# Kernel optimization log

Hardware: AMD Instinct MI355X
Metric: run time of the kernel (lower is better)

## Reference

```python
import jax, jax.numpy as jnp
import numpy as np


def setup_inputs() -> dict:
    key = jax.random.key(0)
    ks = jax.random.split(key, 4)
    B, T, E, H = 4, 4096, 512, 64
    x = jax.random.normal(ks[0], (B, T, E), dtype=jnp.float32)
    s = 1.0 / np.sqrt(E)
    Wq = jax.random.normal(ks[1], (E, H), dtype=jnp.float32) * s
    Wk = jax.random.normal(ks[2], (E, H), dtype=jnp.float32) * s
    Wv = jax.random.normal(ks[3], (E, H), dtype=jnp.float32) * s
    bq = jnp.zeros((H,), dtype=jnp.float32)
    bk = jnp.zeros((H,), dtype=jnp.float32)
    bv = jnp.zeros((H,), dtype=jnp.float32)
    return {"x": x, "Wq": Wq, "bq": bq, "Wk": Wk, "bk": bk, "Wv": Wv, "bv": bv}


def reference(x, Wq, bq, Wk, bk, Wv, bv):
    # Single-head causal attention (masked=True path; dropout off / eval mode).
    B, T, E = x.shape
    H = Wq.shape[1]
    q = x @ Wq + bq                      # [B,T,H]
    k = x @ Wk + bk                      # [B,T,H]
    v = x @ Wv + bv                      # [B,T,H]
    scale = jnp.asarray(H, x.dtype) ** -0.5
    w = jnp.einsum('bqh,bkh->bqk', q, k) * scale   # [B,T,T]
    causal = jnp.tril(jnp.ones((T, T), dtype=bool))
    w = jnp.where(causal, w, jnp.asarray(-jnp.inf, w.dtype))
    w = jax.nn.softmax(w, axis=-1)
    out = jnp.einsum('bqk,bkh->bqh', w, v)          # [B,T,H]
    return out
```

## Files before the change

### kernel.cpp

```cpp
#include <hip/hip_runtime.h>
#include <math.h>

#define B_SZ   4
#define T_SEQ  4096
#define E_DIM  512
#define H_DIM  64
#define AW     8
#define XSTR   520
#define QSCALE 0.180336878f

typedef float f32x4 __attribute__((ext_vector_type(4)));
typedef short s16x4 __attribute__((ext_vector_type(4)));
typedef short s16x8 __attribute__((ext_vector_type(8)));
typedef unsigned int u32x4 __attribute__((ext_vector_type(4)));

static __device__ __forceinline__ unsigned short f2bf(float f) {
    union { float f; unsigned int u; } c; c.f = f;
    return (unsigned short)((c.u + 0x7fffu + ((c.u >> 16) & 1u)) >> 16);
}

static __device__ __forceinline__ float exp2f_hw(float x) {
    return __builtin_amdgcn_exp2f(x);
}

static __device__ __forceinline__ unsigned int pack_bf16(float a, float b) {
    unsigned int ua = __builtin_bit_cast(unsigned int, a) + 0x8000u;
    unsigned int ub = __builtin_bit_cast(unsigned int, b) + 0x8000u;
    return __builtin_amdgcn_perm(ub, ua, 0x07060302u);
}

__global__ __launch_bounds__(256) void wconv(
    const float* __restrict__ Wq, const float* __restrict__ Wk, const float* __restrict__ Wv,
    unsigned short* __restrict__ Wf)
{
    const int fid  = blockIdx.x * 256 + threadIdx.x;
    const int nt   = fid >> 10;
    const int kc32 = (fid >> 6) & 15;
    const int lane = fid & 63;
    const int l15  = lane & 15, g = lane >> 4;
    const int col  = nt * 16 + l15;
    const int m    = col >> 6, h = col & 63;
    const float* src = (m == 0) ? Wq : (m == 1) ? Wk : Wv;
    const float sc = (m == 0) ? QSCALE : 1.0f;
    const int k0 = kc32 * 32 + 4 * g;
    s16x8 o;
    #pragma unroll
    for (int j = 0; j < 4; ++j) {
        o[j]     = (short)f2bf(src[(k0 + j) * H_DIM + h] * sc);
        o[4 + j] = (short)f2bf(src[(k0 + 16 + j) * H_DIM + h] * sc);
    }
    *(s16x8*)(Wf + (long long)fid * 8) = o;
}

__global__ __launch_bounds__(256) void qkv_mfma(
    const float* __restrict__ x, const unsigned short* __restrict__ Wf,
    const float* __restrict__ bq, const float* __restrict__ bk, const float* __restrict__ bv,
    unsigned short* __restrict__ qf, unsigned short* __restrict__ kf,
    unsigned short* __restrict__ vf)
{
    __shared__ unsigned short Xf[16 * XSTR];
    __shared__ unsigned short Wout[192][20];

    const int t = threadIdx.x, wv = t >> 6, l = t & 63, l15 = l & 15, g = l >> 4;
    const long long row0 = (long long)blockIdx.x * 16;

    const float* xbase = x + row0 * E_DIM;
    #pragma unroll
    for (int i = 0; i < 8; ++i) {
        const int n = t + 256 * i;
        const int r = n >> 7;
        const int c = (n & 127) * 4;
        const f32x4 xv = *(const f32x4*)(xbase + r * E_DIM + c);
        const int kc32 = c >> 5, rem = c & 31;
        const int gg = (rem & 15) >> 2, half = rem >> 4;
        unsigned int* dst = (unsigned int*)&Xf[kc32 * XSTR + (r + 16 * gg) * 8 + half * 4];
        dst[0] = pack_bf16(xv[0], xv[1]);
        dst[1] = pack_bf16(xv[2], xv[3]);
    }
    __syncthreads();

    f32x4 acc[3];
    #pragma unroll
    for (int i = 0; i < 3; ++i) acc[i] = (f32x4){0.f, 0.f, 0.f, 0.f};

    #pragma unroll
    for (int kc32 = 0; kc32 < 16; ++kc32) {
        const s16x8 xf = *(const s16x8*)&Xf[kc32 * XSTR + l * 8];
        #pragma unroll
        for (int i = 0; i < 3; ++i) {
            const int nt = wv + 4 * i;
            const s16x8 wf = *(const s16x8*)(Wf + (long long)((nt * 16 + kc32) * 64 + l) * 8);
            acc[i] = __builtin_amdgcn_mfma_f32_16x16x32_bf16(wf, xf, acc[i], 0, 0, 0);
        }
    }

    #pragma unroll
    for (int i = 0; i < 3; ++i) {
        const int nt = wv + 4 * i;
        const float* bsrc = (i == 0) ? bq : (i == 1) ? bk : bv;
        const float bscale = (i == 0) ? QSCALE : 1.0f;
        const f32x4 bb = *(const f32x4*)(bsrc + wv * 16 + 4 * g);
        #pragma unroll
        for (int r = 0; r < 4; ++r)
            Wout[nt * 16 + 4 * g + r][l15] = f2bf(acc[i][r] + bb[r] * bscale);
    }
    __syncthreads();

    const long long qt = blockIdx.x;

    if (t < 128) {
        const int hc = t >> 6, ll = t & 63, p15 = ll & 15, pg = (ll >> 4);
        s16x8 o;
        #pragma unroll
        for (int j = 0; j < 4; ++j) {
            o[j]     = (short)Wout[32 * hc + 4 * pg + j][p15];
            o[4 + j] = (short)Wout[32 * hc + 16 + 4 * pg + j][p15];
        }
        *(s16x8*)(qf + qt * 1024 + hc * 512 + ll * 8) = o;
    } else {
        const int tt = t - 128, half = tt >> 6, ll = tt & 63, p15 = ll & 15, pg = (ll >> 4);
        s16x8 o;
        #pragma unroll
        for (int j = 0; j < 4; ++j) {
            o[j]     = (short)Wout[64 + 32 * half + 4 * pg + j][p15];
            o[4 + j] = (short)Wout[64 + 32 * half + 16 + 4 * pg + j][p15];
        }
        *(s16x8*)(kf + qt * 1024 + half * 512 + ll * 8) = o;
    }

    {
        const int hc = t >> 6, ll = t & 63, p15 = ll & 15, pg = (ll >> 4);
        const long long ktg = qt >> 2;
        const int half = (int)((qt >> 1) & 1), pi = (int)(qt & 1);
        s16x4 o;
        #pragma unroll
        for (int j = 0; j < 4; ++j) o[j] = (short)Wout[128 + hc * 16 + p15][4 * pg + j];
        *(s16x4*)(vf + ktg * 4096 + hc * 1024 + half * 512 + ll * 8 + pi * 4) = o;
    }
}

__global__ __launch_bounds__(512, 2) void attn(
    const unsigned short* __restrict__ qf,
    const unsigned short* __restrict__ kf,
    const unsigned short* __restrict__ vf,
    float* __restrict__ out)
{
    __shared__ float Osh[AW][64][33];
    __shared__ float msh[AW][32];
    __shared__ float lsh[AW][32];

    const int t = threadIdx.x, wv = t >> 6, l = t & 63, l15 = l & 15, g = l >> 4;

    const int bid = blockIdx.x;
    const int xcd = bid & 7;
    const int b   = xcd >> 1;
    const int u   = (bid >> 3) * 2 + (xcd & 1);

    const unsigned short* kfb = kf + (long long)b * 64 * 4096 + l * 8;
    const unsigned short* vfb = vf + (long long)b * 64 * 4096 + l * 8;

    for (int p = 0; p < 2; ++p) {
        const int qi = p ? u : (127 - u);
        const int q0 = qi * 32;
        const int adiag = (q0 + 31) >> 6;

        s16x8 Qf[2][2];
        #pragma unroll
        for (int s = 0; s < 2; ++s) {
            const unsigned short* qp = qf + ((long long)b * 256 + qi * 2 + s) * 1024 + l * 8;
            Qf[s][0] = *(const s16x8*)qp;
            Qf[s][1] = *(const s16x8*)(qp + 512);
        }

        f32x4 O[2][4];
        #pragma unroll
        for (int s = 0; s < 2; ++s)
            #pragma unroll
            for (int hc = 0; hc < 4; ++hc) O[s][hc] = (f32x4){0.f, 0.f, 0.f, 0.f};
        float m[2]   = {-INFINITY, -INFINITY};
        float lsm[2] = {0.f, 0.f};

        s16x8 Ka[4], Kc[4];
        #define LOAD_K(KT, A, C)                                              \
            {                                                                 \
                const unsigned short* p_ = kfb + (long long)(KT) * 4096;      \
                _Pragma("unroll")                                             \
                for (int ks = 0; ks < 4; ++ks) {                              \
                    (A)[ks] = *(const s16x8*)(p_ + ks * 1024);                \
                    (C)[ks] = *(const s16x8*)(p_ + ks * 1024 + 512);          \
                }                                                             \
            }

        if (wv <= adiag) LOAD_K(wv, Ka, Kc);

        for (int kt = wv; kt <= adiag; kt += AW) {
            const int ktb = kt * 64;
            const f32x4 z = {0.f, 0.f, 0.f, 0.f};

            f32x4 S[2][4];
            __builtin_amdgcn_s_setprio(1);
            #pragma unroll
            for (int ks = 0; ks < 4; ++ks) {
                #pragma unroll
                for (int s = 0; s < 2; ++s) {
                    f32x4 s0 = __builtin_amdgcn_mfma_f32_16x16x32_bf16(Ka[ks], Qf[s][0], z, 0, 0, 0);
                    S[s][ks] = __builtin_amdgcn_mfma_f32_16x16x32_bf16(Kc[ks], Qf[s][1], s0, 0, 0, 0);
                }
            }
            __builtin_amdgcn_s_setprio(0);

            s16x8 Va[4], Vc[4];
            {
                const unsigned short* pv = vfb + (long long)kt * 4096;
                #pragma unroll
                for (int hc = 0; hc < 4; ++hc) {
                    Va[hc] = *(const s16x8*)(pv + hc * 1024);
                    Vc[hc] = *(const s16x8*)(pv + hc * 1024 + 512);
                }
            }

            s16x8 Kna[4], Knc[4];
            const int ktn = kt + AW;
            if (ktn <= adiag) LOAD_K(ktn, Kna, Knc);

            if (kt == adiag) {
                #pragma unroll
                for (int s = 0; s < 2; ++s) {
                    const int qg = q0 + 16 * s + l15;
                    #pragma unroll
                    for (int ks = 0; ks < 4; ++ks)
                        #pragma unroll
                        for (int r = 0; r < 4; ++r) {
                            const int key = ktb + 16 * ks + 4 * g + r;
                            S[s][ks][r] = (key > qg) ? -INFINITY : S[s][ks][r];
                        }
                }
            }

            s16x8 Pf[2][2];
            #pragma unroll
            for (int s = 0; s < 2; ++s) {
                float tm = S[s][0][0];
                #pragma unroll
                for (int ks = 0; ks < 4; ++ks)
                    #pragma unroll
                    for (int r = 0; r < 4; ++r) tm = fmaxf(tm, S[s][ks][r]);
                tm = fmaxf(tm, __shfl_xor(tm, 16));
                tm = fmaxf(tm, __shfl_xor(tm, 32));

                if (!__all(tm - m[s] <= 8.f)) {
                    const float mn = fmaxf(m[s], tm);
                    const float alpha = exp2f_hw(m[s] - mn);
                    lsm[s] *= alpha;
                    #pragma unroll
                    for (int hc = 0; hc < 4; ++hc) O[s][hc] *= alpha;
                    m[s] = mn;
                }

                float ps = 0.f;
                #pragma unroll
                for (int ks = 0; ks < 4; ++ks)
                    #pragma unroll
                    for (int r = 0; r < 4; ++r) {
                        const float pp = exp2f_hw(S[s][ks][r] - m[s]);
                        S[s][ks][r] = pp;
                        ps += pp;
                    }
                ps += __shfl_xor(ps, 16);
                ps += __shfl_xor(ps, 32);
                lsm[s] += ps;

                #pragma unroll
                for (int kc = 0; kc < 2; ++kc) {
                    u32x4 w;
                    #pragma unroll
                    for (int i = 0; i < 4; ++i)
                        w[i] = pack_bf16(S[s][2 * kc + (i >> 1)][2 * (i & 1)],
                                         S[s][2 * kc + (i >> 1)][2 * (i & 1) + 1]);
                    Pf[s][kc] = __builtin_bit_cast(s16x8, w);
                }
            }

            __builtin_amdgcn_s_setprio(1);
            #pragma unroll
            for (int hc = 0; hc < 4; ++hc) {
                #pragma unroll
                for (int s = 0; s < 2; ++s) {
                    O[s][hc] = __builtin_amdgcn_mfma_f32_16x16x32_bf16(Va[hc], Pf[s][0], O[s][hc], 0, 0, 0);
                    O[s][hc] = __builtin_amdgcn_mfma_f32_16x16x32_bf16(Vc[hc], Pf[s][1], O[s][hc], 0, 0, 0);
                }
            }
            __builtin_amdgcn_s_setprio(0);

            #pragma unroll
            for (int ks = 0; ks < 4; ++ks) { Ka[ks] = Kna[ks]; Kc[ks] = Knc[ks]; }
        }
        #undef LOAD_K

        #pragma unroll
        for (int s = 0; s < 2; ++s)
            #pragma unroll
            for (int hc = 0; hc < 4; ++hc)
                #pragma unroll
                for (int r = 0; r < 4; ++r)
                    Osh[wv][hc * 16 + 4 * g + r][16 * s + l15] = O[s][hc][r];
        if (g == 0) {
            msh[wv][l15]      = m[0];
            msh[wv][16 + l15] = m[1];
            lsh[wv][l15]      = lsm[0];
            lsh[wv][16 + l15] = lsm[1];
        }
        __syncthreads();

        const int rl = t >> 4;
        const int h0 = (t & 15) * 4;
        float mstar = msh[0][rl];
        #pragma unroll
        for (int w = 1; w < AW; ++w) mstar = fmaxf(mstar, msh[w][rl]);
        float fw[AW], lstar = 0.f;
        #pragma unroll
        for (int w = 0; w < AW; ++w) {
            fw[w] = exp2f_hw(msh[w][rl] - mstar);
            lstar += lsh[w][rl] * fw[w];
        }
        const float inv = 1.f / lstar;

        f32x4 o0;
        #pragma unroll
        for (int j = 0; j < 4; ++j) {
            float a0 = 0.f;
            #pragma unroll
            for (int w = 0; w < AW; ++w) a0 += Osh[w][h0 + j][rl] * fw[w];
            o0[j] = a0 * inv;
        }
        *(f32x4*)(out + ((long long)b * T_SEQ + q0 + rl) * H_DIM + h0) = o0;

        __syncthreads();
    }
}

extern "C" void kernel_launch(void* const* d_in, const int* in_sizes, int n_in,
                              void* d_out, int out_size, void* d_ws, size_t ws_size,
                              hipStream_t stream) {
    const float* x  = (const float*)d_in[0];
    const float* Wq = (const float*)d_in[1];
    const float* bq = (const float*)d_in[2];
    const float* Wk = (const float*)d_in[3];
    const float* bk = (const float*)d_in[4];
    const float* Wv = (const float*)d_in[5];
    const float* bv = (const float*)d_in[6];

    const long long rows = (long long)B_SZ * T_SEQ;
    unsigned short* qfb = (unsigned short*)d_ws;
    unsigned short* kfb = qfb + rows * H_DIM;
    unsigned short* vfb = kfb + rows * H_DIM;
    unsigned short* Wfb = vfb + rows * H_DIM;

    wconv<<<dim3(48), dim3(256), 0, stream>>>(Wq, Wk, Wv, Wfb);
    qkv_mfma<<<dim3(rows / 16), dim3(256), 0, stream>>>(x, Wfb, bq, bk, bv, qfb, kfb, vfb);
    attn<<<dim3(B_SZ * 64), dim3(512), 0, stream>>>(qfb, kfb, vfb, (float*)d_out);
}
```

Baseline: 43.53 us.

## Split attention into one query tile per block; widen QKV tile; defer softmax reductions

The attention kernel now launches twice as many blocks. Each block handles a single 32-row query tile, where before one block processed a long and a short tile in sequence. The softmax loop keeps per-lane partial row sums and reduces them once at the end. The cross-lane max shuffles run only when a rescale is needed. The QKV projection kernel now processes 32 rows per block so that each weight fragment feeds two MFMAs. This trades the earlier pairing-based causal load balance for more parallelism and a shorter critical path per block, and cuts shuffle and weight-load overhead.

```diff
diff --git a/kernel.cpp b/kernel.cpp
--- a/kernel.cpp
+++ b/kernel.cpp
@@ -58,39 +58,44 @@
     unsigned short* __restrict__ qf, unsigned short* __restrict__ kf,
     unsigned short* __restrict__ vf)
 {
-    __shared__ unsigned short Xf[16 * XSTR];
-    __shared__ unsigned short Wout[192][20];
+    __shared__ unsigned short Xf[2][16 * XSTR];
+    __shared__ unsigned short Wout[192][36];
 
     const int t = threadIdx.x, wv = t >> 6, l = t & 63, l15 = l & 15, g = l >> 4;
-    const long long row0 = (long long)blockIdx.x * 16;
+    const long long row0 = (long long)blockIdx.x * 32;
 
     const float* xbase = x + row0 * E_DIM;
     #pragma unroll
-    for (int i = 0; i < 8; ++i) {
+    for (int i = 0; i < 16; ++i) {
         const int n = t + 256 * i;
         const int r = n >> 7;
         const int c = (n & 127) * 4;
         const f32x4 xv = *(const f32x4*)(xbase + r * E_DIM + c);
+        const int rs = r >> 4, rr = r & 15;
         const int kc32 = c >> 5, rem = c & 31;
         const int gg = (rem & 15) >> 2, half = rem >> 4;
-        unsigned int* dst = (unsigned int*)&Xf[kc32 * XSTR + (r + 16 * gg) * 8 + half * 4];
+        unsigned int* dst = (unsigned int*)&Xf[rs][kc32 * XSTR + (rr + 16 * gg) * 8 + half * 4];
         dst[0] = pack_bf16(xv[0], xv[1]);
         dst[1] = pack_bf16(xv[2], xv[3]);
     }
     __syncthreads();
 
-    f32x4 acc[3];
-    #pragma unroll
-    for (int i = 0; i < 3; ++i) acc[i] = (f32x4){0.f, 0.f, 0.f, 0.f};
+    f32x4 acc[2][3];
+    #pragma unroll
+    for (int rs = 0; rs < 2; ++rs)
+        #pragma unroll
+        for (int i = 0; i < 3; ++i) acc[rs][i] = (f32x4){0.f, 0.f, 0.f, 0.f};
 
     #pragma unroll
     for (int kc32 = 0; kc32 < 16; ++kc32) {
-        const s16x8 xf = *(const s16x8*)&Xf[kc32 * XSTR + l * 8];
+        const s16x8 xf0 = *(const s16x8*)&Xf[0][kc32 * XSTR + l * 8];
+        const s16x8 xf1 = *(const s16x8*)&Xf[1][kc32 * XSTR + l * 8];
         #pragma unroll
         for (int i = 0; i < 3; ++i) {
             const int nt = wv + 4 * i;
             const s16x8 wf = *(const s16x8*)(Wf + (long long)((nt * 16 + kc32) * 64 + l) * 8);
-            acc[i] = __builtin_amdgcn_mfma_f32_16x16x32_bf16(wf, xf, acc[i], 0, 0, 0);
+            acc[0][i] = __builtin_amdgcn_mfma_f32_16x16x32_bf16(wf, xf0, acc[0][i], 0, 0, 0);
+            acc[1][i] = __builtin_amdgcn_mfma_f32_16x16x32_bf16(wf, xf1, acc[1][i], 0, 0, 0);
         }
     }
 
@@ -101,41 +106,47 @@
         const float bscale = (i == 0) ? QSCALE : 1.0f;
         const f32x4 bb = *(const f32x4*)(bsrc + wv * 16 + 4 * g);
         #pragma unroll
-        for (int r = 0; r < 4; ++r)
-            Wout[nt * 16 + 4 * g + r][l15] = f2bf(acc[i][r] + bb[r] * bscale);
+        for (int rs = 0; rs < 2; ++rs)
+            #pragma unroll
+            for (int r = 0; r < 4; ++r)
+                Wout[nt * 16 + 4 * g + r][16 * rs + l15] = f2bf(acc[rs][i][r] + bb[r] * bscale);
     }
     __syncthreads();
 
-    const long long qt = blockIdx.x;
-
-    if (t < 128) {
-        const int hc = t >> 6, ll = t & 63, p15 = ll & 15, pg = (ll >> 4);
-        s16x8 o;
-        #pragma unroll
-        for (int j = 0; j < 4; ++j) {
-            o[j]     = (short)Wout[32 * hc + 4 * pg + j][p15];
-            o[4 + j] = (short)Wout[32 * hc + 16 + 4 * pg + j][p15];
-        }
-        *(s16x8*)(qf + qt * 1024 + hc * 512 + ll * 8) = o;
-    } else {
-        const int tt = t - 128, half = tt >> 6, ll = tt & 63, p15 = ll & 15, pg = (ll >> 4);
-        s16x8 o;
-        #pragma unroll
-        for (int j = 0; j < 4; ++j) {
-            o[j]     = (short)Wout[64 + 32 * half + 4 * pg + j][p15];
-            o[4 + j] = (short)Wout[64 + 32 * half + 16 + 4 * pg + j][p15];
-        }
-        *(s16x8*)(kf + qt * 1024 + half * 512 + ll * 8) = o;
-    }
-
-    {
-        const int hc = t >> 6, ll = t & 63, p15 = ll & 15, pg = (ll >> 4);
-        const long long ktg = qt >> 2;
-        const int half = (int)((qt >> 1) & 1), pi = (int)(qt & 1);
-        s16x4 o;
-        #pragma unroll
-        for (int j = 0; j < 4; ++j) o[j] = (short)Wout[128 + hc * 16 + p15][4 * pg + j];
-        *(s16x4*)(vf + ktg * 4096 + hc * 1024 + half * 512 + ll * 8 + pi * 4) = o;
+    #pragma unroll
+    for (int rt = 0; rt < 2; ++rt) {
+        const long long qt = (long long)blockIdx.x * 2 + rt;
+
+        if (t < 128) {
+            const int hc = t >> 6, ll = t & 63, p15 = ll & 15, pg = (ll >> 4);
+            s16x8 o;
+            #pragma unroll
+            for (int j = 0; j < 4; ++j) {
+                o[j]     = (short)Wout[32 * hc + 4 * pg + j][16 * rt + p15];
+                o[4 + j] = (short)Wout[32 * hc + 16 + 4 * pg + j][16 * rt + p15];
+            }
+            *(s16x8*)(qf + qt * 1024 + hc * 512 + ll * 8) = o;
+        } else {
+            const int tt = t - 128, half = tt >> 6, ll = tt & 63, p15 = ll & 15, pg = (ll >> 4);
+            s16x8 o;
+            #pragma unroll
+            for (int j = 0; j < 4; ++j) {
+                o[j]     = (short)Wout[64 + 32 * half + 4 * pg + j][16 * rt + p15];
+                o[4 + j] = (short)Wout[64 + 32 * half + 16 + 4 * pg + j][16 * rt + p15];
+            }
+            *(s16x8*)(kf + qt * 1024 + half * 512 + ll * 8) = o;
+        }
+
+        {
+            const int hc = t >> 6, ll = t & 63, p15 = ll & 15, pg = (ll >> 4);
+            const long long ktg = qt >> 2;
+            const int half = (int)((qt >> 1) & 1), pi = (int)(qt & 1);
+            s16x4 o;
+            #pragma unroll
+            for (int j = 0; j < 4; ++j)
+                o[j] = (short)Wout[128 + hc * 16 + p15][16 * rt + 4 * pg + j];
+            *(s16x4*)(vf + ktg * 4096 + hc * 1024 + half * 512 + ll * 8 + pi * 4) = o;
+        }
     }
 }
 
@@ -155,188 +166,187 @@
     const int xcd = bid & 7;
     const int b   = xcd >> 1;
     const int u   = (bid >> 3) * 2 + (xcd & 1);
+    const int qi  = 127 - u;
+    const int q0  = qi * 32;
+    const int adiag = (q0 + 31) >> 6;
 
     const unsigned short* kfb = kf + (long long)b * 64 * 4096 + l * 8;
     const unsigned short* vfb = vf + (long long)b * 64 * 4096 + l * 8;
 
-    for (int p = 0; p < 2; ++p) {
-        const int qi = p ? u : (127 - u);
-        const int q0 = qi * 32;
-        const int adiag = (q0 + 31) >> 6;
-
-        s16x8 Qf[2][2];
-        #pragma unroll
-        for (int s = 0; s < 2; ++s) {
-            const unsigned short* qp = qf + ((long long)b * 256 + qi * 2 + s) * 1024 + l * 8;
-            Qf[s][0] = *(const s16x8*)qp;
-            Qf[s][1] = *(const s16x8*)(qp + 512);
-        }
-
-        f32x4 O[2][4];
-        #pragma unroll
-        for (int s = 0; s < 2; ++s)
-            #pragma unroll
-            for (int hc = 0; hc < 4; ++hc) O[s][hc] = (f32x4){0.f, 0.f, 0.f, 0.f};
-        float m[2]   = {-INFINITY, -INFINITY};
-        float lsm[2] = {0.f, 0.f};
-
-        s16x8 Ka[4], Kc[4];
-        #define LOAD_K(KT, A, C)                                              \
-            {                                                                 \
-                const unsigned short* p_ = kfb + (long long)(KT) * 4096;      \
-                _Pragma("unroll")                                             \
-                for (int ks = 0; ks < 4; ++ks) {                              \
-                    (A)[ks] = *(const s16x8*)(p_ + ks * 1024);                \
-                    (C)[ks] = *(const s16x8*)(p_ + ks * 1024 + 512);          \
-                }                                                             \
-            }
-
-        if (wv <= adiag) LOAD_K(wv, Ka, Kc);
-
-        for (int kt = wv; kt <= adiag; kt += AW) {
-            const int ktb = kt * 64;
-            const f32x4 z = {0.f, 0.f, 0.f, 0.f};
-
-            f32x4 S[2][4];
-            __builtin_amdgcn_s_setprio(1);
-            #pragma unroll
-            for (int ks = 0; ks < 4; ++ks) {
-                #pragma unroll
-                for (int s = 0; s < 2; ++s) {
-                    f32x4 s0 = __builtin_amdgcn_mfma_f32_16x16x32_bf16(Ka[ks], Qf[s][0], z, 0, 0, 0);
-                    S[s][ks] = __builtin_amdgcn_mfma_f32_16x16x32_bf16(Kc[ks], Qf[s][1], s0, 0, 0, 0);
-                }
-            }
-            __builtin_amdgcn_s_setprio(0);
-
-            s16x8 Va[4], Vc[4];
-            {
-                const unsigned short* pv = vfb + (long long)kt * 4096;
-                #pragma unroll
-                for (int hc = 0; hc < 4; ++hc) {
-                    Va[hc] = *(const s16x8*)(pv + hc * 1024);
-                    Vc[hc] = *(const s16x8*)(pv + hc * 1024 + 512);
-                }
-            }
-
-            s16x8 Kna[4], Knc[4];
-            const int ktn = kt + AW;
-            if (ktn <= adiag) LOAD_K(ktn, Kna, Knc);
-
-            if (kt == adiag) {
-                #pragma unroll
-                for (int s = 0; s < 2; ++s) {
-                    const int qg = q0 + 16 * s + l15;
-                    #pragma unroll
-                    for (int ks = 0; ks < 4; ++ks)
-                        #pragma unroll
-                        for (int r = 0; r < 4; ++r) {
-                            const int key = ktb + 16 * ks + 4 * g + r;
-                            S[s][ks][r] = (key > qg) ? -INFINITY : S[s][ks][r];
-                        }
-                }
-            }
-
-            s16x8 Pf[2][2];
+    s16x8 Qf[2][2];
+    #pragma unroll
+    for (int s = 0; s < 2; ++s) {
+        const unsigned short* qp = qf + ((long long)b * 256 + qi * 2 + s) * 1024 + l * 8;
+        Qf[s][0] = *(const s16x8*)qp;
+        Qf[s][1] = *(const s16x8*)(qp + 512);
+    }
+
+    f32x4 O[2][4];
+    #pragma unroll
+    for (int s = 0; s < 2; ++s)
+        #pragma unroll
+        for (int hc = 0; hc < 4; ++hc) O[s][hc] = (f32x4){0.f, 0.f, 0.f, 0.f};
+    float m[2]   = {-INFINITY, -INFINITY};
+    float lsm[2] = {0.f, 0.f};
+
+    s16x8 Ka[4], Kc[4];
+    #define LOAD_K(KT, A, C)                                              \
+        {                                                                 \
+            const unsigned short* p_ = kfb + (long long)(KT) * 4096;      \
+            _Pragma("unroll")                                             \
+            for (int ks = 0; ks < 4; ++ks) {                              \
+                (A)[ks] = *(const s16x8*)(p_ + ks * 1024);                \
+                (C)[ks] = *(const s16x8*)(p_ + ks * 1024 + 512);          \
+            }                                                             \
+        }
+
+    if (wv <= adiag) LOAD_K(wv, Ka, Kc);
+
+    for (int kt = wv; kt <= adiag; kt += AW) {
+        const int ktb = kt * 64;
+        const f32x4 z = {0.f, 0.f, 0.f, 0.f};
+
+        f32x4 S[2][4];
+        __builtin_amdgcn_s_setprio(1);
+        #pragma unroll
+        for (int ks = 0; ks < 4; ++ks) {
             #pragma unroll
             for (int s = 0; s < 2; ++s) {
-                float tm = S[s][0][0];
-                #pragma unroll
-                for (int ks = 0; ks < 4; ++ks)
-                    #pragma unroll
-                    for (int r = 0; r < 4; ++r) tm = fmaxf(tm, S[s][ks][r]);
-                tm = fmaxf(tm, __shfl_xor(tm, 16));
-                tm = fmaxf(tm, __shfl_xor(tm, 32));
-
-                if (!__all(tm - m[s] <= 8.f)) {
-                    const float mn = fmaxf(m[s], tm);
-                    const float alpha = exp2f_hw(m[s] - mn);
-                    lsm[s] *= alpha;
-                    #pragma unroll
-                    for (int hc = 0; hc < 4; ++hc) O[s][hc] *= alpha;
-                    m[s] = mn;
-                }
-
-                float ps = 0.f;
+                f32x4 s0 = __builtin_amdgcn_mfma_f32_16x16x32_bf16(Ka[ks], Qf[s][0], z, 0, 0, 0);
+                S[s][ks] = __builtin_amdgcn_mfma_f32_16x16x32_bf16(Kc[ks], Qf[s][1], s0, 0, 0, 0);
+            }
+        }
+        __builtin_amdgcn_s_setprio(0);
+
+        s16x8 Va[4], Vc[4];
+        {
+            const unsigned short* pv = vfb + (long long)kt * 4096;
+            #pragma unroll
+            for (int hc = 0; hc < 4; ++hc) {
+                Va[hc] = *(const s16x8*)(pv + hc * 1024);
+                Vc[hc] = *(const s16x8*)(pv + hc * 1024 + 512);
+            }
+        }
+
+        s16x8 Kna[4], Knc[4];
+        const int ktn = kt + AW;
+        if (ktn <= adiag) LOAD_K(ktn, Kna, Knc);
+
+        if (kt == adiag) {
+            #pragma unroll
+            for (int s = 0; s < 2; ++s) {
+                const int qg = q0 + 16 * s + l15;
                 #pragma unroll
                 for (int ks = 0; ks < 4; ++ks)
                     #pragma unroll
                     for (int r = 0; r < 4; ++r) {
-                        const float pp = exp2f_hw(S[s][ks][r] - m[s]);
-                        S[s][ks][r] = pp;
-                        ps += pp;
+                        const int key = ktb + 16 * ks + 4 * g + r;
+                        S[s][ks][r] = (key > qg) ? -INFINITY : S[s][ks][r];
                     }
-                ps += __shfl_xor(ps, 16);
-                ps += __shfl_xor(ps, 32);
-                lsm[s] += ps;
-
-                #pragma unroll
-                for (int kc = 0; kc < 2; ++kc) {
-                    u32x4 w;
-                    #pragma unroll
-                    for (int i = 0; i < 4; ++i)
-                        w[i] = pack_bf16(S[s][2 * kc + (i >> 1)][2 * (i & 1)],
-                                         S[s][2 * kc + (i >> 1)][2 * (i & 1) + 1]);
-                    Pf[s][kc] = __builtin_bit_cast(s16x8, w);
+            }
+        }
+
+        s16x8 Pf[2][2];
+        #pragma unroll
+        for (int s = 0; s < 2; ++s) {
+            float tm = S[s][0][0];
+            #pragma unroll
+            for (int ks = 0; ks < 4; ++ks)
+                #pragma unroll
+                for (int r = 0; r < 4; ++r) tm = fmaxf(tm, S[s][ks][r]);
+
+            if (!__all(tm - m[s] <= 8.f)) {
+                float tr = fmaxf(tm, __shfl_xor(tm, 16));
+                tr = fmaxf(tr, __shfl_xor(tr, 32));
+                const float mn = fmaxf(m[s], tr);
+                const float alpha = exp2f_hw(m[s] - mn);
+                lsm[s] *= alpha;
+                #pragma unroll
+                for (int hc = 0; hc < 4; ++hc) O[s][hc] *= alpha;
+                m[s] = mn;
+            }
+
+            float ps = 0.f;
+            #pragma unroll
+            for (int ks = 0; ks < 4; ++ks)
+                #pragma unroll
+                for (int r = 0; r < 4; ++r) {
+                    const float pp = exp2f_hw(S[s][ks][r] - m[s]);
+                    S[s][ks][r] = pp;
+                    ps += pp;
                 }
-            }
-
-            __builtin_amdgcn_s_setprio(1);
-            #pragma unroll
-            for (int hc = 0; hc < 4; ++hc) {
-                #pragma unroll
-                for (int s = 0; s < 2; ++s) {
-                    O[s][hc] = __builtin_amdgcn_mfma_f32_16x16x32_bf16(Va[hc], Pf[s][0], O[s][hc], 0, 0, 0);
-                    O[s][hc] = __builtin_amdgcn_mfma_f32_16x16x32_bf16(Vc[hc], Pf[s][1], O[s][hc], 0, 0, 0);
-                }
-            }
-            __builtin_amdgcn_s_setprio(0);
-
-            #pragma unroll
-            for (int ks = 0; ks < 4; ++ks) { Ka[ks] = Kna[ks]; Kc[ks] = Knc[ks]; }
-        }
-        #undef LOAD_K
-
-        #pragma unroll
-        for (int s = 0; s < 2; ++s)
-            #pragma unroll
-            for (int hc = 0; hc < 4; ++hc)
-                #pragma unroll
-                for (int r = 0; r < 4; ++r)
-                    Osh[wv][hc * 16 + 4 * g + r][16 * s + l15] = O[s][hc][r];
-        if (g == 0) {
-            msh[wv][l15]      = m[0];
-            msh[wv][16 + l15] = m[1];
-            lsh[wv][l15]      = lsm[0];
-            lsh[wv][16 + l15] = lsm[1];
-        }
-        __syncthreads();
-
-        const int rl = t >> 4;
-        const int h0 = (t & 15) * 4;
-        float mstar = msh[0][rl];
-        #pragma unroll
-        for (int w = 1; w < AW; ++w) mstar = fmaxf(mstar, msh[w][rl]);
-        float fw[AW], lstar = 0.f;
-        #pragma unroll
-        for (int w = 0; w < AW; ++w) {
-            fw[w] = exp2f_hw(msh[w][rl] - mstar);
-            lstar += lsh[w][rl] * fw[w];
-        }
-        const float inv = 1.f / lstar;
-
-        f32x4 o0;
-        #pragma unroll
-        for (int j = 0; j < 4; ++j) {
-            float a0 = 0.f;
-            #pragma unroll
-            for (int w = 0; w < AW; ++w) a0 += Osh[w][h0 + j][rl] * fw[w];
-            o0[j] = a0 * inv;
-        }
-        *(f32x4*)(out + ((long long)b * T_SEQ + q0 + rl) * H_DIM + h0) = o0;
-
-        __syncthreads();
-    }
+            lsm[s] += ps;
+
+            #pragma unroll
+            for (int kc = 0; kc < 2; ++kc) {
+                u32x4 w;
+                #pragma unroll
+                for (int i = 0; i < 4; ++i)
+                    w[i] = pack_bf16(S[s][2 * kc + (i >> 1)][2 * (i & 1)],
+                                     S[s][2 * kc + (i >> 1)][2 * (i & 1) + 1]);
+                Pf[s][kc] = __builtin_bit_cast(s16x8, w);
+            }
+        }
+
+        __builtin_amdgcn_s_setprio(1);
+        #pragma unroll
+        for (int hc = 0; hc < 4; ++hc) {
+            #pragma unroll
+            for (int s = 0; s < 2; ++s) {
+                O[s][hc] = __builtin_amdgcn_mfma_f32_16x16x32_bf16(Va[hc], Pf[s][0], O[s][hc], 0, 0, 0);
+                O[s][hc] = __builtin_amdgcn_mfma_f32_16x16x32_bf16(Vc[hc], Pf[s][1], O[s][hc], 0, 0, 0);
+            }
+        }
+        __builtin_amdgcn_s_setprio(0);
+
+        #pragma unroll
+        for (int ks = 0; ks < 4; ++ks) { Ka[ks] = Kna[ks]; Kc[ks] = Knc[ks]; }
+    }
+    #undef LOAD_K
+
+    #pragma unroll
+    for (int s = 0; s < 2; ++s) {
+        lsm[s] += __shfl_xor(lsm[s], 16);
+        lsm[s] += __shfl_xor(lsm[s], 32);
+    }
+
+    #pragma unroll
+    for (int s = 0; s < 2; ++s)
+        #pragma unroll
+        for (int hc = 0; hc < 4; ++hc)
+            #pragma unroll
+            for (int r = 0; r < 4; ++r)
+                Osh[wv][hc * 16 + 4 * g + r][16 * s + l15] = O[s][hc][r];
+    if (g == 0) {
+        msh[wv][l15]      = m[0];
+        msh[wv][16 + l15] = m[1];
+        lsh[wv][l15]      = lsm[0];
+        lsh[wv][16 + l15] = lsm[1];
+    }
+    __syncthreads();
+
+    const int rl = t >> 4;
+    const int h0 = (t & 15) * 4;
+    float mstar = msh[0][rl];
+    #pragma unroll
+    for (int w = 1; w < AW; ++w) mstar = fmaxf(mstar, msh[w][rl]);
+    float fw[AW], lstar = 0.f;
+    #pragma unroll
+    for (int w = 0; w < AW; ++w) {
+        fw[w] = exp2f_hw(msh[w][rl] - mstar);
+        lstar += lsh[w][rl] * fw[w];
+    }
+    const float inv = 1.f / lstar;
+
+    f32x4 o0;
+    #pragma unroll
+    for (int j = 0; j < 4; ++j) {
+        float a0 = 0.f;
+        #pragma unroll
+        for (int w = 0; w < AW; ++w) a0 += Osh[w][h0 + j][rl] * fw[w];
+        o0[j] = a0 * inv;
+    }
+    *(f32x4*)(out + ((long long)b * T_SEQ + q0 + rl) * H_DIM + h0) = o0;
 }
 
 extern "C" void kernel_launch(void* const* d_in, const int* in_sizes, int n_in,
@@ -357,6 +367,6 @@
     unsigned short* Wfb = vfb + rows * H_DIM;
 
     wconv<<<dim3(48), dim3(256), 0, stream>>>(Wq, Wk, Wv, Wfb);
-    qkv_mfma<<<dim3(rows / 16), dim3(256), 0, stream>>>(x, Wfb, bq, bk, bv, qfb, kfb, vfb);
-    attn<<<dim3(B_SZ * 64), dim3(512), 0, stream>>>(qfb, kfb, vfb, (float*)d_out);
-}
+    qkv_mfma<<<dim3(rows / 32), dim3(256), 0, stream>>>(x, Wfb, bq, bk, bv, qfb, kfb, vfb);
+    attn<<<dim3(B_SZ * 128), dim3(512), 0, stream>>>(qfb, kfb, vfb, (float*)d_out);
+}
```

After: 41.82 us. 1.04x faster.
